# Kernel optimization log

Hardware: AMD Instinct MI355X
Metric: run time of the kernel (lower is better)

The kernel has to match this reference:

```python
import jax, jax.numpy as jnp
import numpy as np

B, S, H, E, V = 128, 128, 1024, 512, 32000

def setup_inputs() -> dict:
    key = jax.random.key(0)
    ks = jax.random.split(key, 14)
    sc = 0.02
    return {
        "x": jax.random.randint(ks[0], (B,), 0, V),
        "hidden": jax.random.normal(ks[1], (1, B, H), jnp.float32),
        "cell": jax.random.normal(ks[2], (1, B, H), jnp.float32),
        "encoder_outputs": jax.random.normal(ks[3], (B, S, H), jnp.float32),
        # parameters
        "emb_table": jax.random.normal(ks[4], (V, E), jnp.float32) * sc,
        "attn_W": jax.random.normal(ks[5], (H, 2 * H), jnp.float32) * sc,
        "attn_b": jnp.zeros((H,), jnp.float32),
        "v": jax.random.uniform(ks[6], (H,), jnp.float32),
        "W_ih": jax.random.normal(ks[7], (4 * H, E + H), jnp.float32) * sc,
        "W_hh": jax.random.normal(ks[8], (4 * H, H), jnp.float32) * sc,
        "b_ih": jnp.zeros((4 * H,), jnp.float32),
        "b_hh": jnp.zeros((4 * H,), jnp.float32),
        "fc_W": jax.random.normal(ks[9], (V, 2 * H), jnp.float32) * sc,
        "fc_b": jnp.zeros((V,), jnp.float32),
    }


def reference(x, hidden, cell, encoder_outputs, emb_table, attn_W, attn_b, v,
              W_ih, W_hh, b_ih, b_hh, fc_W, fc_b):
    b, s, h = encoder_outputs.shape
    h_last = hidden[-1]                      # [B,H]
    c_last = cell[-1]                        # [B,H]

    # Bahdanau attention
    h_rep = jnp.broadcast_to(h_last[:, None, :], (b, s, h))          # [B,S,H]
    cat = jnp.concatenate([h_rep, encoder_outputs], axis=2)          # [B,S,2H]
    energy = jnp.tanh(jnp.einsum('bsk,hk->bsh', cat, attn_W) + attn_b)
    score = jnp.einsum('bsh,h->bs', energy, v)                       # [B,S]
    attn_weights = jax.nn.softmax(score, axis=1)                     # [B,S]
    context = jnp.einsum('bs,bsh->bh', attn_weights, encoder_outputs)  # [B,H]

    # LSTM single step, gate order i,f,g,o (PyTorch convention)
    emb = emb_table[x]                                               # [B,E]
    xin = jnp.concatenate([emb, context], axis=1)                    # [B,E+H]
    gates = xin @ W_ih.T + b_ih + h_last @ W_hh.T + b_hh             # [B,4H]
    i, f, g, o = jnp.split(gates, 4, axis=1)
    c_new = jax.nn.sigmoid(f) * c_last + jax.nn.sigmoid(i) * jnp.tanh(g)
    h_new = jax.nn.sigmoid(o) * jnp.tanh(c_new)

    out = jnp.concatenate([h_new, context], axis=1)                  # [B,2H]
    logits = out @ fc_W.T + fc_b                                     # [B,V]
    return logits, h_new[None], c_new[None], attn_weights
```

## Files before the change

kernel.cpp:

```cpp
#include <hip/hip_runtime.h>
#include <hip/hip_bf16.h>
#include <math.h>

constexpr int B  = 128;
constexpr int S  = 128;
constexpr int H  = 1024;
constexpr int E  = 512;
constexpr int V  = 32000;
constexpr int H2 = 2 * H;
constexpr int G4 = 4 * H;
constexpr int KX = E + H;
constexpr int KG = KX + H;
constexpr int BS = B * S;

typedef float  f32x4  __attribute__((ext_vector_type(4)));
typedef short  short8 __attribute__((ext_vector_type(8)));

__device__ __forceinline__ short f2bf(float f) {
    union { float f; unsigned u; } x; x.f = f;
    unsigned r = (x.u + 0x7FFFu + ((x.u >> 16) & 1u)) >> 16;
    return (short)r;
}
__device__ __forceinline__ float bf2f(unsigned short u) {
    union { unsigned u; float f; } x; x.u = ((unsigned)u) << 16;
    return x.f;
}
__device__ __forceinline__ float fast_tanh(float x) {
    float z = fminf(fmaxf(x, -15.f), 15.f);
    float e = __expf(2.f * z);
    return 1.f - __fdividef(2.f, e + 1.f);
}
__device__ __forceinline__ void glds16(const void* g, void* l) {
    __builtin_amdgcn_global_load_lds(
        (const __attribute__((address_space(1))) unsigned int*)g,
        (__attribute__((address_space(3))) unsigned int*)l,
        16, 0, 0);
}

__global__ __launch_bounds__(256) void k_cvt(const float* __restrict__ enc,
                                             short* __restrict__ encb,
                                             const float* __restrict__ attn_W,
                                             short* __restrict__ w2b) {
    int bid = blockIdx.x;
    if (bid < 16384) {
        size_t p = (size_t)bid * 256 + threadIdx.x;
        float4 a = *(const float4*)(enc + p * 4);
        short4 o = { f2bf(a.x), f2bf(a.y), f2bf(a.z), f2bf(a.w) };
        *(short4*)(encb + p * 4) = o;
    } else {
        int p = (bid - 16384) * 256 + threadIdx.x;
        int row = p >> 8;
        int c = (p & 255) * 4;
        float4 a = *(const float4*)(attn_W + (size_t)row * H2 + H + c);
        short4 o = { f2bf(a.x), f2bf(a.y), f2bf(a.z), f2bf(a.w) };
        *(short4*)(w2b + (size_t)row * H + c) = o;
    }
}

__global__ __launch_bounds__(256) void k_q(const float* __restrict__ hlast,
                                           const float* __restrict__ attn_W,
                                           const float* __restrict__ attn_b,
                                           float* __restrict__ q) {
    int idx = blockIdx.x * 256 + threadIdx.x;
    int b = idx >> 10;
    int h = idx & (H - 1);
    const float* arow = attn_W + (size_t)h * H2;
    const float* hrow = hlast + (size_t)b * H;
    float acc = 0.f;
    for (int k = 0; k < H; k += 4) {
        float4 a = *(const float4*)(arow + k);
        float4 x = *(const float4*)(hrow + k);
        acc += a.x * x.x + a.y * x.y + a.z * x.z + a.w * x.w;
    }
    q[idx] = acc + attn_b[h];
}

__global__ __launch_bounds__(256) void k_energy_mfma(const short* __restrict__ encb,
                                                     const short* __restrict__ w2b,
                                                     const float* __restrict__ q,
                                                     const float* __restrict__ v,
                                                     float* __restrict__ part) {
    __shared__ __align__(16) short A_s[128 * 32];
    __shared__ __align__(16) short B_s[128 * 32];
    __shared__ float red[128][33];

    const int tid  = threadIdx.x;
    const int wave = tid >> 6, lane = tid & 63;
    const int wr = wave >> 1, wc = wave & 1;
    const int c16 = lane & 15, q4 = lane >> 4;
    const int m0 = blockIdx.x * 128;
    const int n0 = blockIdx.y * 128;

    f32x4 acc[4][4] = {};

    const int u0 = wave * 128 + lane;
    const int rowA0 = u0 >> 2,        rowA1 = (u0 + 64) >> 2;
    const int ofsA0 = (u0 & 3) * 8,   ofsA1 = ((u0 + 64) & 3) * 8;
    short* ldsA0 = A_s + wave * 1024;
    short* ldsA1 = A_s + wave * 1024 + 512;
    short* ldsB0 = B_s + wave * 1024;
    short* ldsB1 = B_s + wave * 1024 + 512;
    const short* gA = encb + (size_t)m0 * H;
    const short* gB = w2b + (size_t)n0 * H;

    for (int k0 = 0; k0 < H; k0 += 32) {
        __syncthreads();
        glds16(gA + (size_t)rowA0 * H + k0 + ofsA0, ldsA0);
        glds16(gA + (size_t)rowA1 * H + k0 + ofsA1, ldsA1);
        glds16(gB + (size_t)rowA0 * H + k0 + ofsA0, ldsB0);
        glds16(gB + (size_t)rowA1 * H + k0 + ofsA1, ldsB1);
        __syncthreads();

        short8 a[4], b[4];
#pragma unroll
        for (int i = 0; i < 4; i++)
            a[i] = *(const short8*)(A_s + (wr * 64 + i * 16 + c16) * 32 + q4 * 8);
#pragma unroll
        for (int j = 0; j < 4; j++)
            b[j] = *(const short8*)(B_s + (wc * 64 + j * 16 + c16) * 32 + q4 * 8);
#pragma unroll
        for (int i = 0; i < 4; i++)
#pragma unroll
            for (int j = 0; j < 4; j++)
                acc[i][j] = __builtin_amdgcn_mfma_f32_16x16x32_bf16(a[i], b[j], acc[i][j], 0, 0, 0);
    }

    const float* qb = q + (size_t)blockIdx.x * H;
#pragma unroll
    for (int i = 0; i < 4; i++) {
#pragma unroll
        for (int r = 0; r < 4; r++) {
            float s = 0.f;
#pragma unroll
            for (int j = 0; j < 4; j++) {
                int n = n0 + wc * 64 + j * 16 + c16;
                s += v[n] * fast_tanh(qb[n] + acc[i][j][r]);
            }
            red[wr * 64 + i * 16 + q4 * 4 + r][wc * 16 + c16] = s;
        }
    }
    __syncthreads();
    if (tid < 128) {
        float s = 0.f;
#pragma unroll
        for (int c = 0; c < 32; c++) s += red[tid][c];
        part[(size_t)(m0 + tid) * 8 + blockIdx.y] = s;
    }
}

__global__ __launch_bounds__(256) void k_softmax_ctx(const float* __restrict__ part,
                                                     const short* __restrict__ encb,
                                                     const int* __restrict__ x,
                                                     const float* __restrict__ emb,
                                                     const float* __restrict__ hlast,
                                                     float* __restrict__ attn_out,
                                                     short* __restrict__ xinb) {
    const int b = blockIdx.x;
    const int tid = threadIdx.x;
    __shared__ float w[S];
    __shared__ float red[128];

    float val = 0.f;
    if (tid < S) {
        const float* p = part + (size_t)(b * S + tid) * 8;
#pragma unroll
        for (int t = 0; t < 8; t++) val += p[t];
        w[tid] = val;
        red[tid] = val;
    }
    __syncthreads();
#pragma unroll
    for (int s = 64; s > 0; s >>= 1) {
        if (tid < s) red[tid] = fmaxf(red[tid], red[tid + s]);
        __syncthreads();
    }
    float m = red[0];
    __syncthreads();
    if (tid < S) { val = __expf(w[tid] - m); red[tid] = val; }
    __syncthreads();
#pragma unroll
    for (int s = 64; s > 0; s >>= 1) {
        if (tid < s) red[tid] += red[tid + s];
        __syncthreads();
    }
    float inv = 1.f / red[0];
    if (tid < S) {
        float ww = val * inv;
        w[tid] = ww;
        attn_out[b * S + tid] = ww;
    }
    {
        int xv = x[b];
        float2 e2 = *(const float2*)(emb + (size_t)xv * E + tid * 2);
        short2 eo = { f2bf(e2.x), f2bf(e2.y) };
        *(short2*)(xinb + (size_t)b * KG + tid * 2) = eo;
        float4 h4 = *(const float4*)(hlast + (size_t)b * H + tid * 4);
        short4 ho = { f2bf(h4.x), f2bf(h4.y), f2bf(h4.z), f2bf(h4.w) };
        *(short4*)(xinb + (size_t)b * KG + KX + tid * 4) = ho;
    }
    __syncthreads();

    for (int hb = 0; hb < 2; hb++) {
        int h = hb * 512 + tid * 2;
        const unsigned short* e = (const unsigned short*)encb + (size_t)b * S * H + h;
        float a0 = 0.f, a1 = 0.f;
#pragma unroll 4
        for (int s = 0; s < S; s++) {
            unsigned u = *(const unsigned*)(e + (size_t)s * H);
            float ws_ = w[s];
            a0 += ws_ * bf2f((unsigned short)(u & 0xFFFFu));
            a1 += ws_ * bf2f((unsigned short)(u >> 16));
        }
        short2 o = { f2bf(a0), f2bf(a1) };
        *(short2*)(xinb + (size_t)b * KG + E + h) = o;
    }
}

__global__ __launch_bounds__(256) void k_gates_mfma(const short* __restrict__ xinb,
                                                    const float* __restrict__ W_ih,
                                                    const float* __restrict__ W_hh,
                                                    const float* __restrict__ b_ih,
                                                    const float* __restrict__ b_hh,
                                                    float* __restrict__ gates) {
    __shared__ __align__(16) short A_s[128 * 32];
    __shared__ __align__(16) short B_s[32 * 32];

    const int tid  = threadIdx.x;
    const int wave = tid >> 6, lane = tid & 63;
    const int c16 = lane & 15, q4 = lane >> 4;
    const int n0 = blockIdx.x * 32;

    f32x4 acc[2][2] = {};

    const int u0 = wave * 128 + lane;
    const int rowA0 = u0 >> 2,        rowA1 = (u0 + 64) >> 2;
    const int ofsA0 = (u0 & 3) * 8,   ofsA1 = ((u0 + 64) & 3) * 8;
    short* ldsA0 = A_s + wave * 1024;
    short* ldsA1 = A_s + wave * 1024 + 512;

    const int rB = tid >> 3;
    const int cB = (tid & 7) * 4;

    auto loadB = [&](int k0) -> float4 {
        if (k0 + cB < KX)
            return *(const float4*)(W_ih + (size_t)(n0 + rB) * KX + k0 + cB);
        else
            return *(const float4*)(W_hh + (size_t)(n0 + rB) * H + (k0 - KX) + cB);
    };
    float4 pb = loadB(0);

    for (int k0 = 0; k0 < KG; k0 += 32) {
        __syncthreads();
        short4 wv = { f2bf(pb.x), f2bf(pb.y), f2bf(pb.z), f2bf(pb.w) };
        *(short4*)(B_s + rB * 32 + cB) = wv;
        glds16(xinb + (size_t)rowA0 * KG + k0 + ofsA0, ldsA0);
        glds16(xinb + (size_t)rowA1 * KG + k0 + ofsA1, ldsA1);
        __syncthreads();
        if (k0 + 32 < KG) pb = loadB(k0 + 32);

        short8 a[2], bfr[2];
#pragma unroll
        for (int i = 0; i < 2; i++)
            a[i] = *(const short8*)(A_s + (wave * 32 + i * 16 + c16) * 32 + q4 * 8);
#pragma unroll
        for (int j = 0; j < 2; j++)
            bfr[j] = *(const short8*)(B_s + (j * 16 + c16) * 32 + q4 * 8);
#pragma unroll
        for (int i = 0; i < 2; i++)
#pragma unroll
            for (int j = 0; j < 2; j++)
                acc[i][j] = __builtin_amdgcn_mfma_f32_16x16x32_bf16(a[i], bfr[j], acc[i][j], 0, 0, 0);
    }

#pragma unroll
    for (int i = 0; i < 2; i++)
#pragma unroll
        for (int j = 0; j < 2; j++)
#pragma unroll
            for (int r = 0; r < 4; r++) {
                int R = wave * 32 + i * 16 + q4 * 4 + r;
                int n = n0 + j * 16 + c16;
                gates[(size_t)R * G4 + n] = acc[i][j][r] + b_ih[n] + b_hh[n];
            }
}

__global__ __launch_bounds__(256) void k_lstm(const float* __restrict__ gates,
                                              const float* __restrict__ cell,
                                              const short* __restrict__ xinb,
                                              float* __restrict__ out_h,
                                              float* __restrict__ out_c,
                                              short* __restrict__ xoutb) {
    int idx = blockIdx.x * 256 + threadIdx.x;
    int b = idx >> 10;
    int h = idx & (H - 1);
    const float* g = gates + (size_t)b * G4;
    float ig = g[h], fg = g[H + h], gg = g[2 * H + h], og = g[3 * H + h];
    float si = 1.f / (1.f + expf(-ig));
    float sf = 1.f / (1.f + expf(-fg));
    float so = 1.f / (1.f + expf(-og));
    float c = sf * cell[idx] + si * tanhf(gg);
    float hn = so * tanhf(c);
    out_h[idx] = hn;
    out_c[idx] = c;
    xoutb[(size_t)b * H2 + h] = f2bf(hn);
    xoutb[(size_t)b * H2 + H + h] = xinb[(size_t)b * KG + E + h];
}

__global__ __launch_bounds__(256) void k_fc_mfma(const short* __restrict__ xoutb,
                                                 const float* __restrict__ fcW,
                                                 const float* __restrict__ fcb,
                                                 float* __restrict__ logits) {
    __shared__ __align__(16) short A_s[128 * 32];
    __shared__ __align__(16) short B_s[64 * 32];

    const int tid  = threadIdx.x;
    const int wave = tid >> 6, lane = tid & 63;
    const int wr = wave >> 1, wc = wave & 1;
    const int c16 = lane & 15, q4 = lane >> 4;
    const int n0 = blockIdx.x * 64;

    f32x4 acc[4][2] = {};

    const int u0 = wave * 128 + lane;
    const int rowA0 = u0 >> 2,        rowA1 = (u0 + 64) >> 2;
    const int ofsA0 = (u0 & 3) * 8,   ofsA1 = ((u0 + 64) & 3) * 8;
    short* ldsA0 = A_s + wave * 1024;
    short* ldsA1 = A_s + wave * 1024 + 512;

    const int rB0 = tid >> 3,           rB1 = (tid + 256) >> 3;
    const int cB0 = (tid & 7) * 4;
    const float* gB0 = fcW + (size_t)(n0 + rB0) * H2 + cB0;
    const float* gB1 = fcW + (size_t)(n0 + rB1) * H2 + cB0;

    float4 pb0 = *(const float4*)(gB0);
    float4 pb1 = *(const float4*)(gB1);

    for (int kk = 0; kk < H2 / 32; kk++) {
        const int k0 = kk * 32;
        __syncthreads();
        short4 w0 = { f2bf(pb0.x), f2bf(pb0.y), f2bf(pb0.z), f2bf(pb0.w) };
        short4 w1 = { f2bf(pb1.x), f2bf(pb1.y), f2bf(pb1.z), f2bf(pb1.w) };
        *(short4*)(B_s + rB0 * 32 + cB0) = w0;
        *(short4*)(B_s + rB1 * 32 + cB0) = w1;
        glds16(xoutb + (size_t)rowA0 * H2 + k0 + ofsA0, ldsA0);
        glds16(xoutb + (size_t)rowA1 * H2 + k0 + ofsA1, ldsA1);
        __syncthreads();
        if (kk < H2 / 32 - 1) {
            pb0 = *(const float4*)(gB0 + k0 + 32);
            pb1 = *(const float4*)(gB1 + k0 + 32);
        }

        short8 a[4], b[2];
#pragma unroll
        for (int i = 0; i < 4; i++)
            a[i] = *(const short8*)(A_s + (wr * 64 + i * 16 + c16) * 32 + q4 * 8);
#pragma unroll
        for (int j = 0; j < 2; j++)
            b[j] = *(const short8*)(B_s + (wc * 32 + j * 16 + c16) * 32 + q4 * 8);
#pragma unroll
        for (int i = 0; i < 4; i++)
#pragma unroll
            for (int j = 0; j < 2; j++)
                acc[i][j] = __builtin_amdgcn_mfma_f32_16x16x32_bf16(a[i], b[j], acc[i][j], 0, 0, 0);
    }

#pragma unroll
    for (int i = 0; i < 4; i++)
#pragma unroll
        for (int j = 0; j < 2; j++)
#pragma unroll
            for (int r = 0; r < 4; r++) {
                int R = wr * 64 + i * 16 + q4 * 4 + r;
                int n = n0 + wc * 32 + j * 16 + c16;
                logits[(size_t)R * V + n] = acc[i][j][r] + fcb[n];
            }
}

extern "C" void kernel_launch(void* const* d_in, const int* in_sizes, int n_in,
                              void* d_out, int out_size, void* d_ws, size_t ws_size,
                              hipStream_t stream) {
    const int*   x      = (const int*)d_in[0];
    const float* hidden = (const float*)d_in[1];
    const float* cell   = (const float*)d_in[2];
    const float* enc    = (const float*)d_in[3];
    const float* emb    = (const float*)d_in[4];
    const float* attn_W = (const float*)d_in[5];
    const float* attn_b = (const float*)d_in[6];
    const float* v      = (const float*)d_in[7];
    const float* W_ih   = (const float*)d_in[8];
    const float* W_hh   = (const float*)d_in[9];
    const float* b_ih   = (const float*)d_in[10];
    const float* b_hh   = (const float*)d_in[11];
    const float* fc_W   = (const float*)d_in[12];
    const float* fc_b   = (const float*)d_in[13];

    float* out = (float*)d_out;
    float* logits   = out;
    float* out_h    = out + (size_t)B * V;
    float* out_c    = out_h + (size_t)B * H;
    float* out_attn = out_c + (size_t)B * H;

    char* ws = (char*)d_ws;
    short* encb  = (short*)ws;   ws += (size_t)BS * H * 2;
    short* w2b   = (short*)ws;   ws += (size_t)H * H * 2;
    short* xinb  = (short*)ws;   ws += (size_t)B * KG * 2;
    short* xoutb = (short*)ws;   ws += (size_t)B * H2 * 2;
    float* q     = (float*)ws;   ws += (size_t)B * H * 4;
    float* part  = (float*)ws;   ws += (size_t)BS * 8 * 4;
    float* gates = (float*)ws;   ws += (size_t)B * G4 * 4;

    k_cvt<<<dim3(16384 + 1024), dim3(256), 0, stream>>>(enc, encb, attn_W, w2b);
    k_q<<<dim3(B * H / 256), dim3(256), 0, stream>>>(hidden, attn_W, attn_b, q);
    k_energy_mfma<<<dim3(BS / 128, H / 128), dim3(256), 0, stream>>>(encb, w2b, q, v, part);
    k_softmax_ctx<<<dim3(B), dim3(256), 0, stream>>>(part, encb, x, emb, hidden, out_attn, xinb);
    k_gates_mfma<<<dim3(G4 / 32), dim3(256), 0, stream>>>(xinb, W_ih, W_hh, b_ih, b_hh, gates);
    k_lstm<<<dim3(B * H / 256), dim3(256), 0, stream>>>(gates, cell, xinb, out_h, out_c, xoutb);
    k_fc_mfma<<<dim3(V / 64), dim3(256), 0, stream>>>(xoutb, fc_W, fc_b, logits);
}
```

Before: 714.3 us.

## Fuse q into preprocessing, split softmax-context, split-K gates, LDS-free FC GEMMs

Merges the q projection kernel into the conversion kernel to save a launch. It splits the softmax/context kernel four ways over hidden chunks for more parallelism, and adds split-K over two halves to the gates GEMM, with the partial sums and biases combined in the LSTM kernel. It also rewrites the gates and FC GEMMs to read operands straight from global memory into MFMA fragments, with no LDS staging or block barriers. The cost is redundant softmax computation in each chunk and uncoalesced 16-byte A loads that rely on cache reuse.

```diff
diff --git a/kernel.cpp b/kernel.cpp
--- a/kernel.cpp
+++ b/kernel.cpp
@@ -30,6 +30,12 @@
     float e = __expf(2.f * z);
     return 1.f - __fdividef(2.f, e + 1.f);
 }
+__device__ __forceinline__ short8 cvt8(float4 a, float4 b) {
+    short8 r;
+    r[0] = f2bf(a.x); r[1] = f2bf(a.y); r[2] = f2bf(a.z); r[3] = f2bf(a.w);
+    r[4] = f2bf(b.x); r[5] = f2bf(b.y); r[6] = f2bf(b.z); r[7] = f2bf(b.w);
+    return r;
+}
 __device__ __forceinline__ void glds16(const void* g, void* l) {
     __builtin_amdgcn_global_load_lds(
         (const __attribute__((address_space(1))) unsigned int*)g,
@@ -37,42 +43,40 @@
         16, 0, 0);
 }
 
-__global__ __launch_bounds__(256) void k_cvt(const float* __restrict__ enc,
+__global__ __launch_bounds__(256) void k_pre(const float* __restrict__ enc,
                                              short* __restrict__ encb,
                                              const float* __restrict__ attn_W,
-                                             short* __restrict__ w2b) {
+                                             short* __restrict__ w2b,
+                                             const float* __restrict__ hlast,
+                                             const float* __restrict__ attn_b,
+                                             float* __restrict__ q) {
     int bid = blockIdx.x;
-    if (bid < 16384) {
-        size_t p = (size_t)bid * 256 + threadIdx.x;
+    if (bid < 512) {
+        int idx = bid * 256 + threadIdx.x;
+        int b = idx >> 10;
+        int h = idx & (H - 1);
+        const float* arow = attn_W + (size_t)h * H2;
+        const float* hrow = hlast + (size_t)b * H;
+        float acc = 0.f;
+        for (int k = 0; k < H; k += 4) {
+            float4 a = *(const float4*)(arow + k);
+            float4 x = *(const float4*)(hrow + k);
+            acc += a.x * x.x + a.y * x.y + a.z * x.z + a.w * x.w;
+        }
+        q[idx] = acc + attn_b[h];
+    } else if (bid < 512 + 16384) {
+        size_t p = (size_t)(bid - 512) * 256 + threadIdx.x;
         float4 a = *(const float4*)(enc + p * 4);
         short4 o = { f2bf(a.x), f2bf(a.y), f2bf(a.z), f2bf(a.w) };
         *(short4*)(encb + p * 4) = o;
     } else {
-        int p = (bid - 16384) * 256 + threadIdx.x;
+        int p = (bid - 16896) * 256 + threadIdx.x;
         int row = p >> 8;
         int c = (p & 255) * 4;
         float4 a = *(const float4*)(attn_W + (size_t)row * H2 + H + c);
         short4 o = { f2bf(a.x), f2bf(a.y), f2bf(a.z), f2bf(a.w) };
         *(short4*)(w2b + (size_t)row * H + c) = o;
     }
-}
-
-__global__ __launch_bounds__(256) void k_q(const float* __restrict__ hlast,
-                                           const float* __restrict__ attn_W,
-                                           const float* __restrict__ attn_b,
-                                           float* __restrict__ q) {
-    int idx = blockIdx.x * 256 + threadIdx.x;
-    int b = idx >> 10;
-    int h = idx & (H - 1);
-    const float* arow = attn_W + (size_t)h * H2;
-    const float* hrow = hlast + (size_t)b * H;
-    float acc = 0.f;
-    for (int k = 0; k < H; k += 4) {
-        float4 a = *(const float4*)(arow + k);
-        float4 x = *(const float4*)(hrow + k);
-        acc += a.x * x.x + a.y * x.y + a.z * x.z + a.w * x.w;
-    }
-    q[idx] = acc + attn_b[h];
 }
 
 __global__ __launch_bounds__(256) void k_energy_mfma(const short* __restrict__ encb,
@@ -155,7 +159,8 @@
                                                      const float* __restrict__ hlast,
                                                      float* __restrict__ attn_out,
                                                      short* __restrict__ xinb) {
-    const int b = blockIdx.x;
+    const int bid = blockIdx.x;
+    const int b = bid >> 2, ch = bid & 3;
     const int tid = threadIdx.x;
     __shared__ float w[S];
     __shared__ float red[128];
@@ -185,107 +190,77 @@
     }
     float inv = 1.f / red[0];
     if (tid < S) {
-        float ww = val * inv;
-        w[tid] = ww;
-        attn_out[b * S + tid] = ww;
-    }
-    {
+        val *= inv;
+        w[tid] = val;
+        if (ch == 0) attn_out[b * S + tid] = val;
+    }
+    if (ch == 1) {
         int xv = x[b];
         float2 e2 = *(const float2*)(emb + (size_t)xv * E + tid * 2);
         short2 eo = { f2bf(e2.x), f2bf(e2.y) };
         *(short2*)(xinb + (size_t)b * KG + tid * 2) = eo;
+    } else if (ch == 2) {
         float4 h4 = *(const float4*)(hlast + (size_t)b * H + tid * 4);
         short4 ho = { f2bf(h4.x), f2bf(h4.y), f2bf(h4.z), f2bf(h4.w) };
         *(short4*)(xinb + (size_t)b * KG + KX + tid * 4) = ho;
     }
     __syncthreads();
 
-    for (int hb = 0; hb < 2; hb++) {
-        int h = hb * 512 + tid * 2;
-        const unsigned short* e = (const unsigned short*)encb + (size_t)b * S * H + h;
-        float a0 = 0.f, a1 = 0.f;
-#pragma unroll 4
-        for (int s = 0; s < S; s++) {
-            unsigned u = *(const unsigned*)(e + (size_t)s * H);
-            float ws_ = w[s];
-            a0 += ws_ * bf2f((unsigned short)(u & 0xFFFFu));
-            a1 += ws_ * bf2f((unsigned short)(u >> 16));
-        }
-        short2 o = { f2bf(a0), f2bf(a1) };
-        *(short2*)(xinb + (size_t)b * KG + E + h) = o;
-    }
-}
-
-__global__ __launch_bounds__(256) void k_gates_mfma(const short* __restrict__ xinb,
-                                                    const float* __restrict__ W_ih,
-                                                    const float* __restrict__ W_hh,
-                                                    const float* __restrict__ b_ih,
-                                                    const float* __restrict__ b_hh,
-                                                    float* __restrict__ gates) {
-    __shared__ __align__(16) short A_s[128 * 32];
-    __shared__ __align__(16) short B_s[32 * 32];
-
+    const int h = ch * 256 + tid;
+    const unsigned short* e = (const unsigned short*)encb + (size_t)b * S * H + h;
+    float a0 = 0.f;
+#pragma unroll 8
+    for (int s = 0; s < S; s++) a0 += w[s] * bf2f(e[(size_t)s * H]);
+    xinb[(size_t)b * KG + E + h] = f2bf(a0);
+}
+
+__global__ __launch_bounds__(128) void k_gates_direct(const short* __restrict__ xinb,
+                                                      const float* __restrict__ W_ih,
+                                                      const float* __restrict__ W_hh,
+                                                      float* __restrict__ gpart) {
     const int tid  = threadIdx.x;
     const int wave = tid >> 6, lane = tid & 63;
     const int c16 = lane & 15, q4 = lane >> 4;
-    const int n0 = blockIdx.x * 32;
-
-    f32x4 acc[2][2] = {};
-
-    const int u0 = wave * 128 + lane;
-    const int rowA0 = u0 >> 2,        rowA1 = (u0 + 64) >> 2;
-    const int ofsA0 = (u0 & 3) * 8,   ofsA1 = ((u0 + 64) & 3) * 8;
-    short* ldsA0 = A_s + wave * 1024;
-    short* ldsA1 = A_s + wave * 1024 + 512;
-
-    const int rB = tid >> 3;
-    const int cB = (tid & 7) * 4;
-
-    auto loadB = [&](int k0) -> float4 {
-        if (k0 + cB < KX)
-            return *(const float4*)(W_ih + (size_t)(n0 + rB) * KX + k0 + cB);
-        else
-            return *(const float4*)(W_hh + (size_t)(n0 + rB) * H + (k0 - KX) + cB);
+    const int n = blockIdx.x * 32 + wave * 16 + c16;
+    const int kh = blockIdx.y;
+    const int kbeg = kh * (KG / 2), kend = kbeg + (KG / 2);
+
+    const short* arow = xinb + (size_t)c16 * KG;
+
+    auto bptr = [&](int k) -> const float* {
+        return (k < KX) ? (W_ih + (size_t)n * KX + k)
+                        : (W_hh + (size_t)n * H + (k - KX));
     };
-    float4 pb = loadB(0);
-
-    for (int k0 = 0; k0 < KG; k0 += 32) {
-        __syncthreads();
-        short4 wv = { f2bf(pb.x), f2bf(pb.y), f2bf(pb.z), f2bf(pb.w) };
-        *(short4*)(B_s + rB * 32 + cB) = wv;
-        glds16(xinb + (size_t)rowA0 * KG + k0 + ofsA0, ldsA0);
-        glds16(xinb + (size_t)rowA1 * KG + k0 + ofsA1, ldsA1);
-        __syncthreads();
-        if (k0 + 32 < KG) pb = loadB(k0 + 32);
-
-        short8 a[2], bfr[2];
-#pragma unroll
-        for (int i = 0; i < 2; i++)
-            a[i] = *(const short8*)(A_s + (wave * 32 + i * 16 + c16) * 32 + q4 * 8);
-#pragma unroll
-        for (int j = 0; j < 2; j++)
-            bfr[j] = *(const short8*)(B_s + (j * 16 + c16) * 32 + q4 * 8);
-#pragma unroll
-        for (int i = 0; i < 2; i++)
-#pragma unroll
-            for (int j = 0; j < 2; j++)
-                acc[i][j] = __builtin_amdgcn_mfma_f32_16x16x32_bf16(a[i], bfr[j], acc[i][j], 0, 0, 0);
-    }
-
-#pragma unroll
-    for (int i = 0; i < 2; i++)
-#pragma unroll
-        for (int j = 0; j < 2; j++)
-#pragma unroll
-            for (int r = 0; r < 4; r++) {
-                int R = wave * 32 + i * 16 + q4 * 4 + r;
-                int n = n0 + j * 16 + c16;
-                gates[(size_t)R * G4 + n] = acc[i][j][r] + b_ih[n] + b_hh[n];
-            }
-}
-
-__global__ __launch_bounds__(256) void k_lstm(const float* __restrict__ gates,
+
+    f32x4 acc[8] = {};
+    float4 p0 = *(const float4*)bptr(kbeg + q4 * 8);
+    float4 p1 = *(const float4*)bptr(kbeg + q4 * 8 + 4);
+
+    for (int k0 = kbeg; k0 < kend; k0 += 32) {
+        short8 bfr = cvt8(p0, p1);
+        if (k0 + 32 < kend) {
+            p0 = *(const float4*)bptr(k0 + 32 + q4 * 8);
+            p1 = *(const float4*)bptr(k0 + 32 + q4 * 8 + 4);
+        }
+#pragma unroll
+        for (int i = 0; i < 8; i++) {
+            short8 a = *(const short8*)(arow + (size_t)i * 16 * KG + k0 + q4 * 8);
+            acc[i] = __builtin_amdgcn_mfma_f32_16x16x32_bf16(a, bfr, acc[i], 0, 0, 0);
+        }
+    }
+
+    float* gp = gpart + (size_t)kh * B * G4;
+#pragma unroll
+    for (int i = 0; i < 8; i++)
+#pragma unroll
+        for (int r = 0; r < 4; r++)
+            gp[(size_t)(i * 16 + q4 * 4 + r) * G4 + n] = acc[i][r];
+}
+
+__global__ __launch_bounds__(256) void k_lstm(const float* __restrict__ gpart,
                                               const float* __restrict__ cell,
+                                              const float* __restrict__ b_ih,
+                                              const float* __restrict__ b_hh,
                                               const short* __restrict__ xinb,
                                               float* __restrict__ out_h,
                                               float* __restrict__ out_c,
@@ -293,8 +268,12 @@
     int idx = blockIdx.x * 256 + threadIdx.x;
     int b = idx >> 10;
     int h = idx & (H - 1);
-    const float* g = gates + (size_t)b * G4;
-    float ig = g[h], fg = g[H + h], gg = g[2 * H + h], og = g[3 * H + h];
+    const float* g0 = gpart + (size_t)b * G4;
+    const float* g1 = gpart + (size_t)B * G4 + (size_t)b * G4;
+    float ig = g0[h]         + g1[h]         + b_ih[h]         + b_hh[h];
+    float fg = g0[H + h]     + g1[H + h]     + b_ih[H + h]     + b_hh[H + h];
+    float gg = g0[2 * H + h] + g1[2 * H + h] + b_ih[2 * H + h] + b_hh[2 * H + h];
+    float og = g0[3 * H + h] + g1[3 * H + h] + b_ih[3 * H + h] + b_hh[3 * H + h];
     float si = 1.f / (1.f + expf(-ig));
     float sf = 1.f / (1.f + expf(-fg));
     float so = 1.f / (1.f + expf(-og));
@@ -306,74 +285,54 @@
     xoutb[(size_t)b * H2 + H + h] = xinb[(size_t)b * KG + E + h];
 }
 
-__global__ __launch_bounds__(256) void k_fc_mfma(const short* __restrict__ xoutb,
-                                                 const float* __restrict__ fcW,
-                                                 const float* __restrict__ fcb,
-                                                 float* __restrict__ logits) {
-    __shared__ __align__(16) short A_s[128 * 32];
-    __shared__ __align__(16) short B_s[64 * 32];
-
+__global__ __launch_bounds__(256) void k_fc_direct(const short* __restrict__ xoutb,
+                                                   const float* __restrict__ fcW,
+                                                   const float* __restrict__ fcb,
+                                                   float* __restrict__ logits) {
     const int tid  = threadIdx.x;
     const int wave = tid >> 6, lane = tid & 63;
-    const int wr = wave >> 1, wc = wave & 1;
     const int c16 = lane & 15, q4 = lane >> 4;
-    const int n0 = blockIdx.x * 64;
-
-    f32x4 acc[4][2] = {};
-
-    const int u0 = wave * 128 + lane;
-    const int rowA0 = u0 >> 2,        rowA1 = (u0 + 64) >> 2;
-    const int ofsA0 = (u0 & 3) * 8,   ofsA1 = ((u0 + 64) & 3) * 8;
-    short* ldsA0 = A_s + wave * 1024;
-    short* ldsA1 = A_s + wave * 1024 + 512;
-
-    const int rB0 = tid >> 3,           rB1 = (tid + 256) >> 3;
-    const int cB0 = (tid & 7) * 4;
-    const float* gB0 = fcW + (size_t)(n0 + rB0) * H2 + cB0;
-    const float* gB1 = fcW + (size_t)(n0 + rB1) * H2 + cB0;
-
-    float4 pb0 = *(const float4*)(gB0);
-    float4 pb1 = *(const float4*)(gB1);
-
-    for (int kk = 0; kk < H2 / 32; kk++) {
-        const int k0 = kk * 32;
-        __syncthreads();
-        short4 w0 = { f2bf(pb0.x), f2bf(pb0.y), f2bf(pb0.z), f2bf(pb0.w) };
-        short4 w1 = { f2bf(pb1.x), f2bf(pb1.y), f2bf(pb1.z), f2bf(pb1.w) };
-        *(short4*)(B_s + rB0 * 32 + cB0) = w0;
-        *(short4*)(B_s + rB1 * 32 + cB0) = w1;
-        glds16(xoutb + (size_t)rowA0 * H2 + k0 + ofsA0, ldsA0);
-        glds16(xoutb + (size_t)rowA1 * H2 + k0 + ofsA1, ldsA1);
-        __syncthreads();
-        if (kk < H2 / 32 - 1) {
-            pb0 = *(const float4*)(gB0 + k0 + 32);
-            pb1 = *(const float4*)(gB1 + k0 + 32);
-        }
-
-        short8 a[4], b[2];
-#pragma unroll
-        for (int i = 0; i < 4; i++)
-            a[i] = *(const short8*)(A_s + (wr * 64 + i * 16 + c16) * 32 + q4 * 8);
-#pragma unroll
-        for (int j = 0; j < 2; j++)
-            b[j] = *(const short8*)(B_s + (wc * 32 + j * 16 + c16) * 32 + q4 * 8);
-#pragma unroll
-        for (int i = 0; i < 4; i++)
-#pragma unroll
-            for (int j = 0; j < 2; j++)
-                acc[i][j] = __builtin_amdgcn_mfma_f32_16x16x32_bf16(a[i], b[j], acc[i][j], 0, 0, 0);
-    }
-
-#pragma unroll
-    for (int i = 0; i < 4; i++)
-#pragma unroll
-        for (int j = 0; j < 2; j++)
-#pragma unroll
-            for (int r = 0; r < 4; r++) {
-                int R = wr * 64 + i * 16 + q4 * 4 + r;
-                int n = n0 + wc * 32 + j * 16 + c16;
-                logits[(size_t)R * V + n] = acc[i][j][r] + fcb[n];
-            }
+    const int n = blockIdx.x * 64 + wave * 16 + c16;
+
+    const float* brow = fcW + (size_t)n * H2;
+    const short* arow = xoutb + (size_t)c16 * H2;
+
+    f32x4 acc[8] = {};
+
+    float4 a0 = *(const float4*)(brow + q4 * 8);
+    float4 a1 = *(const float4*)(brow + q4 * 8 + 4);
+    float4 b0 = *(const float4*)(brow + 32 + q4 * 8);
+    float4 b1 = *(const float4*)(brow + 32 + q4 * 8 + 4);
+
+    for (int k0 = 0; k0 < H2; k0 += 64) {
+        short8 bfA = cvt8(a0, a1);
+        if (k0 + 64 < H2) {
+            a0 = *(const float4*)(brow + k0 + 64 + q4 * 8);
+            a1 = *(const float4*)(brow + k0 + 64 + q4 * 8 + 4);
+        }
+#pragma unroll
+        for (int i = 0; i < 8; i++) {
+            short8 a = *(const short8*)(arow + (size_t)i * 16 * H2 + k0 + q4 * 8);
+            acc[i] = __builtin_amdgcn_mfma_f32_16x16x32_bf16(a, bfA, acc[i], 0, 0, 0);
+        }
+        short8 bfB = cvt8(b0, b1);
+        if (k0 + 96 < H2) {
+            b0 = *(const float4*)(brow + k0 + 96 + q4 * 8);
+            b1 = *(const float4*)(brow + k0 + 96 + q4 * 8 + 4);
+        }
+#pragma unroll
+        for (int i = 0; i < 8; i++) {
+            short8 a = *(const short8*)(arow + (size_t)i * 16 * H2 + k0 + 32 + q4 * 8);
+            acc[i] = __builtin_amdgcn_mfma_f32_16x16x32_bf16(a, bfB, acc[i], 0, 0, 0);
+        }
+    }
+
+    const float bias = fcb[n];
+#pragma unroll
+    for (int i = 0; i < 8; i++)
+#pragma unroll
+        for (int r = 0; r < 4; r++)
+            logits[(size_t)(i * 16 + q4 * 4 + r) * V + n] = acc[i][r] + bias;
 }
 
 extern "C" void kernel_launch(void* const* d_in, const int* in_sizes, int n_in,
@@ -407,13 +366,14 @@
     short* xoutb = (short*)ws;   ws += (size_t)B * H2 * 2;
     float* q     = (float*)ws;   ws += (size_t)B * H * 4;
     float* part  = (float*)ws;   ws += (size_t)BS * 8 * 4;
-    float* gates = (float*)ws;   ws += (size_t)B * G4 * 4;
-
-    k_cvt<<<dim3(16384 + 1024), dim3(256), 0, stream>>>(enc, encb, attn_W, w2b);
-    k_q<<<dim3(B * H / 256), dim3(256), 0, stream>>>(hidden, attn_W, attn_b, q);
+    float* gpart = (float*)ws;   ws += (size_t)2 * B * G4 * 4;
+
+    k_pre<<<dim3(512 + 16384 + 1024), dim3(256), 0, stream>>>(enc, encb, attn_W, w2b,
+                                                              hidden, attn_b, q);
     k_energy_mfma<<<dim3(BS / 128, H / 128), dim3(256), 0, stream>>>(encb, w2b, q, v, part);
-    k_softmax_ctx<<<dim3(B), dim3(256), 0, stream>>>(part, encb, x, emb, hidden, out_attn, xinb);
-    k_gates_mfma<<<dim3(G4 / 32), dim3(256), 0, stream>>>(xinb, W_ih, W_hh, b_ih, b_hh, gates);
-    k_lstm<<<dim3(B * H / 256), dim3(256), 0, stream>>>(gates, cell, xinb, out_h, out_c, xoutb);
-    k_fc_mfma<<<dim3(V / 64), dim3(256), 0, stream>>>(xoutb, fc_W, fc_b, logits);
-}
+    k_softmax_ctx<<<dim3(B * 4), dim3(256), 0, stream>>>(part, encb, x, emb, hidden, out_attn, xinb);
+    k_gates_direct<<<dim3(G4 / 32, 2), dim3(128), 0, stream>>>(xinb, W_ih, W_hh, gpart);
+    k_lstm<<<dim3(B * H / 256), dim3(256), 0, stream>>>(gpart, cell, b_ih, b_hh, xinb,
+                                                        out_h, out_c, xoutb);
+    k_fc_direct<<<dim3(V / 64), dim3(256), 0, stream>>>(xoutb, fc_W, fc_b, logits);
+}
```

Measured after the change: 732.1 us. 1.02x slower.
